# Optimization experiments

Hardware: AMD Instinct MI355X
Metric: run time of the kernel (lower is better)

Reference implementation:

```python
import jax, jax.numpy as jnp
import numpy as np

D_MODEL = 1024
N_HEADS = 16
DEPTH = D_MODEL // N_HEADS
B, S = 2, 2048
EPS_LN = 1e-6
EPS_KL = 2e-8


def _dense(x, W, b):
    return x @ W + b


def _ln(x, g, b):
    mu = jnp.mean(x, axis=-1, keepdims=True)
    var = jnp.mean(jnp.square(x - mu), axis=-1, keepdims=True)
    return (x - mu) * jax.lax.rsqrt(var + EPS_LN) * g + b


def _split_heads(x):
    # (B,S,D_MODEL) -> (B,H,S,DEPTH)
    return x.reshape(B, S, N_HEADS, DEPTH).transpose(0, 2, 1, 3)


def setup_inputs() -> dict:
    key = jax.random.key(0)
    ks = jax.random.split(key, 12)
    sc = 1.0 / np.sqrt(D_MODEL)
    inp = {
        'q_in': jax.random.normal(ks[0], (B, S, D_MODEL), jnp.float32),
        'k_in': jax.random.normal(ks[1], (B, S, D_MODEL), jnp.float32),
        'Wq': jax.random.normal(ks[2], (D_MODEL, D_MODEL), jnp.float32) * sc,
        'bq': jnp.zeros((D_MODEL,), jnp.float32),
        'Wk': jax.random.normal(ks[3], (D_MODEL, D_MODEL), jnp.float32) * sc,
        'bk': jnp.zeros((D_MODEL,), jnp.float32),
        'Wv': jax.random.normal(ks[4], (D_MODEL, D_MODEL), jnp.float32) * sc,
        'bv': jnp.zeros((D_MODEL,), jnp.float32),
        'Wo': jax.random.normal(ks[5], (D_MODEL, D_MODEL), jnp.float32) * sc,
        'bo': jnp.zeros((D_MODEL,), jnp.float32),
        'g1': jnp.ones((D_MODEL,), jnp.float32), 'b1': jnp.zeros((D_MODEL,), jnp.float32),
        'g2': jnp.ones((D_MODEL,), jnp.float32), 'b2': jnp.zeros((D_MODEL,), jnp.float32),
        'g3': jnp.ones((D_MODEL,), jnp.float32), 'b3': jnp.zeros((D_MODEL,), jnp.float32),
    }
    return inp


def reference(q_in, k_in, Wq, bq, Wk, bk, Wv, bv, Wo, bo, g1, b1, g2, b2, g3, b3):
    # Faithful to source: Wq applied twice to q, Wk twice to k, v = Wv(Wk(k_in))
    q = _ln(_dense(_dense(q_in, Wq, bq), Wq, bq), g1, b1)
    k1 = _dense(k_in, Wk, bk)
    k = _ln(_dense(k1, Wk, bk), g2, b2)
    v = _ln(_dense(k1, Wv, bv), g3, b3)

    q = _split_heads(q)   # (B,H,S,DEPTH)
    k = _split_heads(k)
    v = _split_heads(v)

    # KL-divergence attention scores.
    q_prob = jax.nn.softmax(q, axis=-1)
    k_prob = jax.nn.softmax(k, axis=-1)
    # sum_d q_prob*(log q_prob - log(k_prob+eps))
    # = [sum_d q_prob*log q_prob] - q_prob @ log(k_prob+eps)^T  (no 5D tensor)
    ent = jnp.sum(q_prob * jnp.log(q_prob), axis=-1)                     # (B,H,Sq)
    cross = jnp.einsum('bhqd,bhkd->bhqk', q_prob, jnp.log(k_prob + EPS_KL))
    kl_scores = ent[..., None] - cross                                   # (B,H,Sq,Sk)
    logits = kl_scores / jnp.sqrt(jnp.float32(DEPTH))

    # Csch softmax: csch(x)/sum csch(x)
    csch = 1.0 / jnp.sinh(logits)
    attn = csch / jnp.sum(csch, axis=-1, keepdims=True)                  # (B,H,Sq,Sk)

    out = jnp.einsum('bhqk,bhkd->bhqd', attn, v)
    out = out.transpose(0, 2, 1, 3).reshape(B, S, D_MODEL)
    output = _dense(out, Wo, bo)
    return output, attn
```

## Files before the change

kernel.cpp:

```cpp
#include <hip/hip_runtime.h>
#include <cstddef>
#include <cstdint>

#define BS      2
#define SEQ     2048
#define DM      1024
#define NH      16
#define DEPTH   64
#define ROWS    (BS*SEQ)
#define BHS     (BS*NH*SEQ)

typedef unsigned short u16;
typedef __attribute__((ext_vector_type(8))) short short8v;
typedef __attribute__((ext_vector_type(4))) float f32x4;

#define SWZ(row, cb) ((((row) << 7)) | ((cb) ^ (((row) & 7) << 4)))

__device__ __forceinline__ u16 f2bf(float x) {
    unsigned u = __builtin_bit_cast(unsigned, x);
    unsigned r = u + 0x7FFFu + ((u >> 16) & 1u);
    return (u16)(r >> 16);
}
__device__ __forceinline__ float bf2f(u16 h) {
    unsigned u = ((unsigned)h) << 16;
    return __builtin_bit_cast(float, u);
}

__device__ __forceinline__ float fast_csch(float x) {
    float t    = __expf(x);
    float den  = fmaf(t, t, -1.0f);
    bool  sm   = fabsf(x) < 0.04f;
    float d    = sm ? x : den;
    float r    = __builtin_amdgcn_rcpf(d);
    float big  = 2.0f * t * r;
    float smal = fmaf(x, -(1.0f/6.0f), r);
    return sm ? smal : big;
}

__global__ __launch_bounds__(256) void wsplit_kernel(
    const float* __restrict__ W, u16* __restrict__ H, u16* __restrict__ L)
{
    __shared__ float tile[32][33];
    const int bn = blockIdx.x, bk = blockIdx.y;
    const int c = threadIdx.x & 31, r0 = threadIdx.x >> 5;
#pragma unroll
    for (int r = 0; r < 32; r += 8)
        tile[r0 + r][c] = W[(size_t)(bk*32 + r0 + r) * DM + bn*32 + c];
    __syncthreads();
#pragma unroll
    for (int r = 0; r < 32; r += 8) {
        float v = tile[c][r0 + r];
        u16 h = f2bf(v);
        size_t o = (size_t)(bn*32 + r0 + r) * DM + bk*32 + c;
        H[o] = h;
        L[o] = f2bf(v - bf2f(h));
    }
}

__global__ __launch_bounds__(256) void split_kernel(
    const float* __restrict__ X, u16* __restrict__ H, u16* __restrict__ L)
{
    int i = blockIdx.x * 256 + threadIdx.x;
    float4 v = ((const float4*)X)[i];
    u16 h0 = f2bf(v.x), h1 = f2bf(v.y), h2 = f2bf(v.z), h3 = f2bf(v.w);
    u16 l0 = f2bf(v.x - bf2f(h0)), l1 = f2bf(v.y - bf2f(h1));
    u16 l2 = f2bf(v.z - bf2f(h2)), l3 = f2bf(v.w - bf2f(h3));
    uint2 hh, ll;
    hh.x = (unsigned)h0 | ((unsigned)h1 << 16); hh.y = (unsigned)h2 | ((unsigned)h3 << 16);
    ll.x = (unsigned)l0 | ((unsigned)l1 << 16); ll.y = (unsigned)l2 | ((unsigned)l3 << 16);
    ((uint2*)H)[i] = hh;
    ((uint2*)L)[i] = ll;
}

template<int OUT_MODE>
__global__ __launch_bounds__(256) void gemm_mfma(
    const u16* __restrict__ Ah, const u16* __restrict__ Al,
    const u16* __restrict__ Bh, const u16* __restrict__ Bl,
    const float* __restrict__ bias, float* __restrict__ C,
    u16* __restrict__ Ch, u16* __restrict__ Cl)
{
    constexpr int K = 1024, N = 1024;
    __shared__ u16 AsH[128*40], AsL[128*40], BsH[64*40], BsL[64*40];

    const int t = threadIdx.x;
    const int m0 = blockIdx.y * 128;
    const int n0 = blockIdx.x * 64;
    const int lane = t & 63, w = t >> 6;
    const int wr = w >> 1, wc = w & 1;
    const int lr = lane & 15, lk = lane >> 4;

    f32x4 acc[4][2];
#pragma unroll
    for (int i = 0; i < 4; ++i)
#pragma unroll
        for (int j = 0; j < 2; ++j) acc[i][j] = (f32x4){0.f,0.f,0.f,0.f};

    for (int k0 = 0; k0 < K; k0 += 32) {
        __syncthreads();
#pragma unroll
        for (int r = 0; r < 2; ++r) {
            int s = r*256 + t;
            int row = s >> 2, c = s & 3;
            size_t g = (size_t)(m0 + row) * K + k0 + c*8;
            *(short8v*)&AsH[row*40 + c*8] = *(const short8v*)&Ah[g];
            *(short8v*)&AsL[row*40 + c*8] = *(const short8v*)&Al[g];
        }
        {
            int row = t >> 2, c = t & 3;
            size_t g = (size_t)(n0 + row) * K + k0 + c*8;
            *(short8v*)&BsH[row*40 + c*8] = *(const short8v*)&Bh[g];
            *(short8v*)&BsL[row*40 + c*8] = *(const short8v*)&Bl[g];
        }
        __syncthreads();

        short8v ah[4], al[4], bh[2], bl[2];
#pragma unroll
        for (int i = 0; i < 4; ++i) {
            int off = (wr*64 + i*16 + lr)*40 + lk*8;
            ah[i] = *(const short8v*)&AsH[off];
            al[i] = *(const short8v*)&AsL[off];
        }
#pragma unroll
        for (int j = 0; j < 2; ++j) {
            int off = (wc*32 + j*16 + lr)*40 + lk*8;
            bh[j] = *(const short8v*)&BsH[off];
            bl[j] = *(const short8v*)&BsL[off];
        }
        __builtin_amdgcn_s_setprio(1);
#pragma unroll
        for (int i = 0; i < 4; ++i)
#pragma unroll
            for (int j = 0; j < 2; ++j) {
                acc[i][j] = __builtin_amdgcn_mfma_f32_16x16x32_bf16(ah[i], bh[j], acc[i][j], 0, 0, 0);
                acc[i][j] = __builtin_amdgcn_mfma_f32_16x16x32_bf16(ah[i], bl[j], acc[i][j], 0, 0, 0);
                acc[i][j] = __builtin_amdgcn_mfma_f32_16x16x32_bf16(al[i], bh[j], acc[i][j], 0, 0, 0);
            }
        __builtin_amdgcn_s_setprio(0);
    }

    float bj[2];
#pragma unroll
    for (int j = 0; j < 2; ++j) bj[j] = bias[n0 + wc*32 + j*16 + lr];
#pragma unroll
    for (int i = 0; i < 4; ++i)
#pragma unroll
        for (int j = 0; j < 2; ++j) {
            int col = n0 + wc*32 + j*16 + lr;
#pragma unroll
            for (int r = 0; r < 4; ++r) {
                int row = m0 + wr*64 + i*16 + lk*4 + r;
                float v = acc[i][j][r] + bj[j];
                size_t o = (size_t)row * N + col;
                if constexpr (OUT_MODE == 0) {
                    C[o] = v;
                } else {
                    u16 h = f2bf(v);
                    Ch[o] = h;
                    Cl[o] = f2bf(v - bf2f(h));
                }
            }
        }
}

template<int MODE>
__global__ __launch_bounds__(256) void ln_head_kernel(
    const float* __restrict__ X, const float* __restrict__ G,
    const float* __restrict__ Bt, u16* __restrict__ OA,
    u16* __restrict__ OB, float* __restrict__ ENT)
{
    const int row = blockIdx.x;
    const int tid = threadIdx.x;
    const float* x = X + (size_t)row * DM;
    float4 v = *(const float4*)&x[tid*4];

    float s  = v.x + v.y + v.z + v.w;
    float ss = v.x*v.x + v.y*v.y + v.z*v.z + v.w*v.w;
#pragma unroll
    for (int m = 1; m < 64; m <<= 1) { s += __shfl_xor(s, m); ss += __shfl_xor(ss, m); }
    __shared__ float redS[4], redQ[4];
    const int wave = tid >> 6, lane = tid & 63;
    if (lane == 0) { redS[wave] = s; redQ[wave] = ss; }
    __syncthreads();
    s  = redS[0] + redS[1] + redS[2] + redS[3];
    ss = redQ[0] + redQ[1] + redQ[2] + redQ[3];
    const float mu   = s * (1.0f / DM);
    const float var  = ss * (1.0f / DM) - mu * mu;
    const float rsig = rsqrtf(var + 1e-6f);

    float4 gv = *(const float4*)&G[tid*4];
    float4 bv = *(const float4*)&Bt[tid*4];
    float y0 = (v.x - mu) * rsig * gv.x + bv.x;
    float y1 = (v.y - mu) * rsig * gv.y + bv.y;
    float y2 = (v.z - mu) * rsig * gv.z + bv.z;
    float y3 = (v.w - mu) * rsig * gv.w + bv.w;

    const int b  = row >> 11;
    const int sl = row & (SEQ - 1);
    const int h  = tid >> 4;
    const size_t obase = (((size_t)(b*NH + h)) * SEQ + sl) * DEPTH + (tid & 15) * 4;

    if constexpr (MODE == 2) {
        unsigned w0 = (unsigned)f2bf(y0) | ((unsigned)f2bf(y1) << 16);
        unsigned w1 = (unsigned)f2bf(y2) | ((unsigned)f2bf(y3) << 16);
        *(uint2*)&OA[obase] = make_uint2(w0, w1);
    } else {
        float mx = fmaxf(fmaxf(y0, y1), fmaxf(y2, y3));
#pragma unroll
        for (int m = 1; m < 16; m <<= 1) mx = fmaxf(mx, __shfl_xor(mx, m, 16));
        float e0 = expf(y0 - mx), e1 = expf(y1 - mx), e2 = expf(y2 - mx), e3 = expf(y3 - mx);
        float se = e0 + e1 + e2 + e3;
#pragma unroll
        for (int m = 1; m < 16; m <<= 1) se += __shfl_xor(se, m, 16);
        float inv = 1.0f / se;
        float p0 = e0*inv, p1 = e1*inv, p2 = e2*inv, p3 = e3*inv;
        float o0, o1, o2, o3;
        if constexpr (MODE == 0) { o0 = p0; o1 = p1; o2 = p2; o3 = p3; }
        else {
            o0 = logf(p0 + 2e-8f); o1 = logf(p1 + 2e-8f);
            o2 = logf(p2 + 2e-8f); o3 = logf(p3 + 2e-8f);
        }
        u16 h0 = f2bf(o0), h1 = f2bf(o1), h2 = f2bf(o2), h3 = f2bf(o3);
        unsigned w0 = (unsigned)h0 | ((unsigned)h1 << 16);
        unsigned w1 = (unsigned)h2 | ((unsigned)h3 << 16);
        *(uint2*)&OA[obase] = make_uint2(w0, w1);
        u16 l0 = f2bf(o0 - bf2f(h0)), l1 = f2bf(o1 - bf2f(h1));
        u16 l2 = f2bf(o2 - bf2f(h2)), l3 = f2bf(o3 - bf2f(h3));
        w0 = (unsigned)l0 | ((unsigned)l1 << 16);
        w1 = (unsigned)l2 | ((unsigned)l3 << 16);
        *(uint2*)&OB[obase] = make_uint2(w0, w1);

        if constexpr (MODE == 0) {
            float lse = logf(se);
            float el = p0*(y0-mx-lse) + p1*(y1-mx-lse) + p2*(y2-mx-lse) + p3*(y3-mx-lse);
#pragma unroll
            for (int m = 1; m < 16; m <<= 1) el += __shfl_xor(el, m, 16);
            if ((tid & 15) == 0) ENT[((size_t)(b*NH + h)) * SEQ + sl] = el;
        }
    }
}

__global__ __launch_bounds__(256) void vtrans_kernel(
    const u16* __restrict__ Vb, u16* __restrict__ VT)
{
    __shared__ u16 T[256*72];
    const int bh = blockIdx.y;
    const int s0 = blockIdx.x * 256;
    const int t  = threadIdx.x;
#pragma unroll
    for (int i = 0; i < 8; ++i) {
        int c = i*256 + t;
        int s = c >> 3, d0 = (c & 7) * 8;
        *(short8v*)&T[s*72 + d0] =
            *(const short8v*)&Vb[((size_t)bh*SEQ + s0 + s)*DEPTH + d0];
    }
    __syncthreads();
#pragma unroll
    for (int i = 0; i < 8; ++i) {
        int c = i*256 + t;
        int d = c >> 5, sl0 = (c & 31) * 8;
        short8v v;
#pragma unroll
        for (int j = 0; j < 8; ++j) v[j] = (short)T[(sl0 + j)*72 + d];
        *(short8v*)&VT[((size_t)bh*DEPTH + d)*SEQ + s0 + sl0] = v;
    }
}

__global__ __launch_bounds__(256, 4) void attn5_kernel(
    const u16* __restrict__ QPh, const u16* __restrict__ QPl,
    const u16* __restrict__ LKh, const u16* __restrict__ LKl,
    const u16* __restrict__ VT, const float* __restrict__ ENT,
    float* __restrict__ ATTN, u16* __restrict__ OH, u16* __restrict__ OL)
{
    const int wg   = blockIdx.x;
    const int wgid = (wg & 7) * 128 + (wg >> 3);
    const int bh   = wgid >> 5;
    const int q0   = (wgid & 31) * 64;

    const int t  = threadIdx.x;
    const int l  = t & 63, w = t >> 6;
    const int lr = l & 15, lg = l >> 4;
    const size_t rbase = (size_t)bh * SEQ;

    __shared__ u16 KhS[64*64], KlS[64*64], VtS[64*64], PS[64*64];

    short8v qh[2], ql[2];
#pragma unroll
    for (int d = 0; d < 2; ++d) {
        size_t g = (rbase + q0 + w*16 + lr) * DEPTH + d*32 + lg*8;
        qh[d] = *(const short8v*)&QPh[g];
        ql[d] = *(const short8v*)&QPl[g];
    }
    float e8[4];
#pragma unroll
    for (int r = 0; r < 4; ++r)
        e8[r] = ENT[rbase + q0 + w*16 + lg*4 + r] * 0.125f;

    float rs[4] = {0.f, 0.f, 0.f, 0.f};
    for (int k0 = 0; k0 < SEQ; k0 += 64) {
        if (k0) __syncthreads();
#pragma unroll
        for (int r = 0; r < 2; ++r) {
            int s = r*256 + t; int kr = s >> 3, cb = (s & 7) * 16;
            size_t g = (rbase + k0 + kr) * DEPTH + (s & 7) * 8;
            *(short8v*)((char*)KhS + SWZ(kr, cb)) = *(const short8v*)&LKh[g];
            *(short8v*)((char*)KlS + SWZ(kr, cb)) = *(const short8v*)&LKl[g];
        }
        __syncthreads();

        f32x4 acc[4];
#pragma unroll
        for (int f = 0; f < 4; ++f) acc[f] = (f32x4){0.f,0.f,0.f,0.f};
        __builtin_amdgcn_s_setprio(1);
#pragma unroll
        for (int f = 0; f < 4; ++f)
#pragma unroll
            for (int d = 0; d < 2; ++d) {
                int off = SWZ(f*16 + lr, d*64 + lg*16);
                short8v kbh = *(const short8v*)((const char*)KhS + off);
                short8v kbl = *(const short8v*)((const char*)KlS + off);
                acc[f] = __builtin_amdgcn_mfma_f32_16x16x32_bf16(qh[d], kbh, acc[f], 0, 0, 0);
                acc[f] = __builtin_amdgcn_mfma_f32_16x16x32_bf16(qh[d], kbl, acc[f], 0, 0, 0);
                acc[f] = __builtin_amdgcn_mfma_f32_16x16x32_bf16(ql[d], kbh, acc[f], 0, 0, 0);
            }
        __builtin_amdgcn_s_setprio(0);
#pragma unroll
        for (int f = 0; f < 4; ++f)
#pragma unroll
            for (int r = 0; r < 4; ++r)
                rs[r] += fast_csch(fmaf(acc[f][r], -0.125f, e8[r]));
    }
#pragma unroll
    for (int m = 1; m < 16; m <<= 1)
#pragma unroll
        for (int r = 0; r < 4; ++r) rs[r] += __shfl_xor(rs[r], m, 16);
    float inv[4];
#pragma unroll
    for (int r = 0; r < 4; ++r) inv[r] = 1.0f / rs[r];

    f32x4 av[4];
#pragma unroll
    for (int nf = 0; nf < 4; ++nf) av[nf] = (f32x4){0.f,0.f,0.f,0.f};

    for (int k0 = 0; k0 < SEQ; k0 += 64) {
        __syncthreads();
#pragma unroll
        for (int r = 0; r < 2; ++r) {
            int s = r*256 + t; int kr = s >> 3, cb = (s & 7) * 16;
            size_t g = (rbase + k0 + kr) * DEPTH + (s & 7) * 8;
            *(short8v*)((char*)KhS + SWZ(kr, cb)) = *(const short8v*)&LKh[g];
            *(short8v*)((char*)KlS + SWZ(kr, cb)) = *(const short8v*)&LKl[g];
        }
#pragma unroll
        for (int r = 0; r < 2; ++r) {
            int s = r*256 + t; int dd = s >> 3, cb = (s & 7) * 16;
            *(short8v*)((char*)VtS + SWZ(dd, cb)) =
                *(const short8v*)&VT[((size_t)bh * DEPTH + dd) * SEQ + k0 + (s & 7) * 8];
        }
        __syncthreads();

        f32x4 acc[4];
#pragma unroll
        for (int f = 0; f < 4; ++f) acc[f] = (f32x4){0.f,0.f,0.f,0.f};
        __builtin_amdgcn_s_setprio(1);
#pragma unroll
        for (int f = 0; f < 4; ++f)
#pragma unroll
            for (int d = 0; d < 2; ++d) {
                int off = SWZ(f*16 + lr, d*64 + lg*16);
                short8v kbh = *(const short8v*)((const char*)KhS + off);
                short8v kbl = *(const short8v*)((const char*)KlS + off);
                acc[f] = __builtin_amdgcn_mfma_f32_16x16x32_bf16(qh[d], kbh, acc[f], 0, 0, 0);
                acc[f] = __builtin_amdgcn_mfma_f32_16x16x32_bf16(qh[d], kbl, acc[f], 0, 0, 0);
                acc[f] = __builtin_amdgcn_mfma_f32_16x16x32_bf16(ql[d], kbh, acc[f], 0, 0, 0);
            }
        __builtin_amdgcn_s_setprio(0);

#pragma unroll
        for (int f = 0; f < 4; ++f)
#pragma unroll
            for (int r = 0; r < 4; ++r) {
                float c = fast_csch(fmaf(acc[f][r], -0.125f, e8[r]));
                float a = c * inv[r];
                int q = w*16 + lg*4 + r;
                ATTN[(rbase + q0 + q) * SEQ + k0 + f*16 + lr] = a;
                *(u16*)((char*)PS + SWZ(q, (f*16 + lr)*2)) = f2bf(a);
            }

        short8v pa[2];
#pragma unroll
        for (int ks = 0; ks < 2; ++ks)
            pa[ks] = *(const short8v*)((const char*)PS + SWZ(w*16 + lr, ks*64 + lg*16));
        __builtin_amdgcn_s_setprio(1);
#pragma unroll
        for (int nf = 0; nf < 4; ++nf)
#pragma unroll
            for (int ks = 0; ks < 2; ++ks) {
                short8v vb = *(const short8v*)((const char*)VtS + SWZ(nf*16 + lr, ks*64 + lg*16));
                av[nf] = __builtin_amdgcn_mfma_f32_16x16x32_bf16(pa[ks], vb, av[nf], 0, 0, 0);
            }
        __builtin_amdgcn_s_setprio(0);
    }

    const int b = bh >> 4, h = bh & (NH - 1);
#pragma unroll
    for (int nf = 0; nf < 4; ++nf)
#pragma unroll
        for (int r = 0; r < 4; ++r) {
            int q = w*16 + lg*4 + r;
            int d = nf*16 + lr;
            size_t o = ((size_t)(b * SEQ + q0 + q)) * DM + h * DEPTH + d;
            float v = av[nf][r];
            u16 hh = f2bf(v);
            OH[o] = hh;
            OL[o] = f2bf(v - bf2f(hh));
        }
}

extern "C" void kernel_launch(void* const* d_in, const int* in_sizes, int n_in,
                              void* d_out, int out_size, void* d_ws, size_t ws_size,
                              hipStream_t stream)
{
    const float* q_in = (const float*)d_in[0];
    const float* k_in = (const float*)d_in[1];
    const float* Wq = (const float*)d_in[2];
    const float* bq = (const float*)d_in[3];
    const float* Wk = (const float*)d_in[4];
    const float* bk = (const float*)d_in[5];
    const float* Wv = (const float*)d_in[6];
    const float* bvp = (const float*)d_in[7];
    const float* Wo = (const float*)d_in[8];
    const float* bo = (const float*)d_in[9];
    const float* g1 = (const float*)d_in[10];
    const float* b1 = (const float*)d_in[11];
    const float* g2 = (const float*)d_in[12];
    const float* b2 = (const float*)d_in[13];
    const float* g3 = (const float*)d_in[14];
    const float* b3 = (const float*)d_in[15];

    float* out0 = (float*)d_out;
    float* attn = out0 + (size_t)ROWS * DM;

    char* base = (char*)d_ws;
    const size_t SLOT = (size_t)ROWS * DM * 4;
    const size_t HALF = (size_t)ROWS * DM;
    float* S0f = (float*)(base);
    float* S1f = (float*)(base + SLOT);
    float* S2f = (float*)(base + 2*SLOT);
    float* S3f = (float*)(base + 3*SLOT);
    u16* S0h = (u16*)S0f; u16* S0l = S0h + HALF;
    u16* S1h = (u16*)S1f; u16* S1l = S1h + HALF;
    u16* S3h = (u16*)S3f; u16* S3l = S3h + HALF;
    u16* QPh = (u16*)S3f; u16* QPl = QPh + HALF;
    u16* LKh = (u16*)S2f; u16* LKl = LKh + HALF;
    u16* Vb  = (u16*)S0f; u16* VTp = Vb + HALF;
    u16* OHp = (u16*)S1f; u16* OLp = OHp + HALF;

    char* wbase = base + 4*SLOT;
    const size_t WSZ = (size_t)DM * DM * 2;
    u16* WqH = (u16*)(wbase);           u16* WqL = (u16*)(wbase + WSZ);
    u16* WkH = (u16*)(wbase + 2*WSZ);   u16* WkL = (u16*)(wbase + 3*WSZ);
    u16* WvH = (u16*)(wbase + 4*WSZ);   u16* WvL = (u16*)(wbase + 5*WSZ);
    u16* WoH = (u16*)(wbase + 6*WSZ);   u16* WoL = (u16*)(wbase + 7*WSZ);
    float* ent = (float*)(wbase + 8*WSZ);

    const dim3 wgrid(32, 32);
    const dim3 ggrid(DM/64, ROWS/128);

    wsplit_kernel<<<wgrid, 256, 0, stream>>>(Wq, WqH, WqL);
    wsplit_kernel<<<wgrid, 256, 0, stream>>>(Wk, WkH, WkL);
    wsplit_kernel<<<wgrid, 256, 0, stream>>>(Wv, WvH, WvL);
    wsplit_kernel<<<wgrid, 256, 0, stream>>>(Wo, WoH, WoL);

    split_kernel<<<ROWS*DM/(4*256), 256, 0, stream>>>(q_in, S0h, S0l);
    gemm_mfma<1><<<ggrid, 256, 0, stream>>>(S0h, S0l, WqH, WqL, bq, nullptr, S1h, S1l);
    gemm_mfma<0><<<ggrid, 256, 0, stream>>>(S1h, S1l, WqH, WqL, bq, S2f, nullptr, nullptr);
    split_kernel<<<ROWS*DM/(4*256), 256, 0, stream>>>(k_in, S0h, S0l);
    gemm_mfma<1><<<ggrid, 256, 0, stream>>>(S0h, S0l, WkH, WkL, bk, nullptr, S3h, S3l);
    gemm_mfma<0><<<ggrid, 256, 0, stream>>>(S3h, S3l, WkH, WkL, bk, S0f, nullptr, nullptr);
    gemm_mfma<0><<<ggrid, 256, 0, stream>>>(S3h, S3l, WvH, WvL, bvp, S1f, nullptr, nullptr);

    ln_head_kernel<0><<<ROWS, 256, 0, stream>>>(S2f, g1, b1, QPh, QPl, ent);
    ln_head_kernel<1><<<ROWS, 256, 0, stream>>>(S0f, g2, b2, LKh, LKl, nullptr);
    ln_head_kernel<2><<<ROWS, 256, 0, stream>>>(S1f, g3, b3, Vb, nullptr, nullptr);
    vtrans_kernel<<<dim3(SEQ/256, BS*NH), 256, 0, stream>>>(Vb, VTp);

    attn5_kernel<<<dim3(SEQ/64 * BS*NH), 256, 0, stream>>>(
        QPh, QPl, LKh, LKl, VTp, ent, attn, OHp, OLp);

    gemm_mfma<0><<<ggrid, 256, 0, stream>>>(OHp, OLp, WoH, WoL, bo, out0, nullptr, nullptr);
}
```

Baseline: 581.2 us.

## Precompose Wq·Wq, fuse input splitting into GEMM, prefetch attention K/V tiles

Computes Wq@Wq and the folded bias once, so the double q projection becomes a single GEMM over a 1024x1024 weight product. A new GEMM variant loads fp32 activations and splits them into bf16 hi/lo inside the kernel, which removes the separate split passes. The four weight-split launches are merged into one launch, and the attention kernel now prefetches the next K/Kl/V tile into registers while computing the current one. In exchange it adds a small GEMM and a bias kernel, raises register pressure in attention, and changes rounding order in the q path.

```diff
diff --git a/kernel.cpp b/kernel.cpp
--- a/kernel.cpp
+++ b/kernel.cpp
@@ -37,9 +37,19 @@
     return sm ? smal : big;
 }
 
-__global__ __launch_bounds__(256) void wsplit_kernel(
-    const float* __restrict__ W, u16* __restrict__ H, u16* __restrict__ L)
-{
+__global__ __launch_bounds__(256) void wsplit4_kernel(
+    const float* __restrict__ W0, const float* __restrict__ W1,
+    const float* __restrict__ W2_, const float* __restrict__ W3,
+    u16* __restrict__ H0, u16* __restrict__ L0, u16* __restrict__ H1, u16* __restrict__ L1,
+    u16* __restrict__ H2, u16* __restrict__ L2, u16* __restrict__ H3, u16* __restrict__ L3)
+{
+    const float* W; u16* H; u16* L;
+    switch (blockIdx.z) {
+        case 0: W = W0; H = H0; L = L0; break;
+        case 1: W = W1; H = H1; L = L1; break;
+        case 2: W = W2_; H = H2; L = L2; break;
+        default: W = W3; H = H3; L = L3; break;
+    }
     __shared__ float tile[32][33];
     const int bn = blockIdx.x, bk = blockIdx.y;
     const int c = threadIdx.x & 31, r0 = threadIdx.x >> 5;
@@ -72,6 +82,25 @@
     ((uint2*)L)[i] = ll;
 }
 
+__global__ __launch_bounds__(256) void bias2_kernel(
+    const float* __restrict__ bq, const float* __restrict__ Wq,
+    float* __restrict__ bq2)
+{
+    __shared__ float part[4][64];
+    const int t = threadIdx.x;
+    const int nl = t & 63, kk = t >> 6;
+    const int n = blockIdx.x * 64 + nl;
+    float acc = 0.0f;
+#pragma unroll 8
+    for (int k = kk*256; k < kk*256 + 256; ++k)
+        acc = fmaf(bq[k], Wq[(size_t)k * DM + n], acc);
+    part[kk][nl] = acc;
+    __syncthreads();
+    if (t < 64)
+        bq2[blockIdx.x*64 + t] = part[0][t] + part[1][t] + part[2][t] + part[3][t]
+                               + bq[blockIdx.x*64 + t];
+}
+
 template<int OUT_MODE>
 __global__ __launch_bounds__(256) void gemm_mfma(
     const u16* __restrict__ Ah, const u16* __restrict__ Al,
@@ -140,7 +169,7 @@
 
     float bj[2];
 #pragma unroll
-    for (int j = 0; j < 2; ++j) bj[j] = bias[n0 + wc*32 + j*16 + lr];
+    for (int j = 0; j < 2; ++j) bj[j] = bias ? bias[n0 + wc*32 + j*16 + lr] : 0.0f;
 #pragma unroll
     for (int i = 0; i < 4; ++i)
 #pragma unroll
@@ -162,6 +191,106 @@
         }
 }
 
+template<int OUT_MODE>
+__global__ __launch_bounds__(256) void gemm_f32a(
+    const float* __restrict__ A,
+    const u16* __restrict__ Bh, const u16* __restrict__ Bl,
+    const float* __restrict__ bias, float* __restrict__ C,
+    u16* __restrict__ Ch, u16* __restrict__ Cl)
+{
+    constexpr int K = 1024, N = 1024;
+    __shared__ u16 AsH[128*40], AsL[128*40], BsH[64*40], BsL[64*40];
+
+    const int t = threadIdx.x;
+    const int m0 = blockIdx.y * 128;
+    const int n0 = blockIdx.x * 64;
+    const int lane = t & 63, w = t >> 6;
+    const int wr = w >> 1, wc = w & 1;
+    const int lr = lane & 15, lk = lane >> 4;
+
+    f32x4 acc[4][2];
+#pragma unroll
+    for (int i = 0; i < 4; ++i)
+#pragma unroll
+        for (int j = 0; j < 2; ++j) acc[i][j] = (f32x4){0.f,0.f,0.f,0.f};
+
+    for (int k0 = 0; k0 < K; k0 += 32) {
+        __syncthreads();
+#pragma unroll
+        for (int r = 0; r < 2; ++r) {
+            int j = r*256 + t;
+            int row = j >> 2, c8 = j & 3;
+            const float* src = &A[(size_t)(m0 + row) * K + k0 + c8*8];
+            float4 a = *(const float4*)src;
+            float4 b = *(const float4*)(src + 4);
+            float xs[8] = {a.x,a.y,a.z,a.w,b.x,b.y,b.z,b.w};
+            short8v hv, lv;
+#pragma unroll
+            for (int jj = 0; jj < 8; ++jj) {
+                u16 h = f2bf(xs[jj]);
+                hv[jj] = (short)h;
+                lv[jj] = (short)f2bf(xs[jj] - bf2f(h));
+            }
+            *(short8v*)&AsH[row*40 + c8*8] = hv;
+            *(short8v*)&AsL[row*40 + c8*8] = lv;
+        }
+        {
+            int row = t >> 2, c = t & 3;
+            size_t g = (size_t)(n0 + row) * K + k0 + c*8;
+            *(short8v*)&BsH[row*40 + c*8] = *(const short8v*)&Bh[g];
+            *(short8v*)&BsL[row*40 + c*8] = *(const short8v*)&Bl[g];
+        }
+        __syncthreads();
+
+        short8v ah[4], al[4], bh[2], bl[2];
+#pragma unroll
+        for (int i = 0; i < 4; ++i) {
+            int off = (wr*64 + i*16 + lr)*40 + lk*8;
+            ah[i] = *(const short8v*)&AsH[off];
+            al[i] = *(const short8v*)&AsL[off];
+        }
+#pragma unroll
+        for (int j = 0; j < 2; ++j) {
+            int off = (wc*32 + j*16 + lr)*40 + lk*8;
+            bh[j] = *(const short8v*)&BsH[off];
+            bl[j] = *(const short8v*)&BsL[off];
+        }
+        __builtin_amdgcn_s_setprio(1);
+#pragma unroll
+        for (int i = 0; i < 4; ++i)
+#pragma unroll
+            for (int j = 0; j < 2; ++j) {
+                acc[i][j] = __builtin_amdgcn_mfma_f32_16x16x32_bf16(ah[i], bh[j], acc[i][j], 0, 0, 0);
+                acc[i][j] = __builtin_amdgcn_mfma_f32_16x16x32_bf16(ah[i], bl[j], acc[i][j], 0, 0, 0);
+                acc[i][j] = __builtin_amdgcn_mfma_f32_16x16x32_bf16(al[i], bh[j], acc[i][j], 0, 0, 0);
+            }
+        __builtin_amdgcn_s_setprio(0);
+    }
+
+    float bj[2];
+#pragma unroll
+    for (int j = 0; j < 2; ++j) bj[j] = bias ? bias[n0 + wc*32 + j*16 + lr] : 0.0f;
+#pragma unroll
+    for (int i = 0; i < 4; ++i)
+#pragma unroll
+        for (int j = 0; j < 2; ++j) {
+            int col = n0 + wc*32 + j*16 + lr;
+#pragma unroll
+            for (int r = 0; r < 4; ++r) {
+                int row = m0 + wr*64 + i*16 + lk*4 + r;
+                float v = acc[i][j][r] + bj[j];
+                size_t o = (size_t)row * N + col;
+                if constexpr (OUT_MODE == 0) {
+                    C[o] = v;
+                } else {
+                    u16 h = f2bf(v);
+                    Ch[o] = h;
+                    Cl[o] = f2bf(v - bf2f(h));
+                }
+            }
+        }
+}
+
 template<int MODE>
 __global__ __launch_bounds__(256) void ln_head_kernel(
     const float* __restrict__ X, const float* __restrict__ G,
@@ -265,7 +394,7 @@
     }
 }
 
-__global__ __launch_bounds__(256, 4) void attn5_kernel(
+__global__ __launch_bounds__(256, 4) void attn6_kernel(
     const u16* __restrict__ QPh, const u16* __restrict__ QPl,
     const u16* __restrict__ LKh, const u16* __restrict__ LKl,
     const u16* __restrict__ VT, const float* __restrict__ ENT,
@@ -283,6 +412,10 @@
 
     __shared__ u16 KhS[64*64], KlS[64*64], VtS[64*64], PS[64*64];
 
+    const int kr0 = t >> 3,           c0 = t & 7;
+    const int kr1 = (256 + t) >> 3,   c1 = t & 7;
+    const int wz0 = SWZ(kr0, c0*16), wz1 = SWZ(kr1, c1*16);
+
     short8v qh[2], ql[2];
 #pragma unroll
     for (int d = 0; d < 2; ++d) {
@@ -295,17 +428,26 @@
     for (int r = 0; r < 4; ++r)
         e8[r] = ENT[rbase + q0 + w*16 + lg*4 + r] * 0.125f;
 
+    {
+        size_t g0 = (rbase + kr0) * DEPTH + c0*8;
+        size_t g1 = (rbase + kr1) * DEPTH + c1*8;
+        *(short8v*)((char*)KhS + wz0) = *(const short8v*)&LKh[g0];
+        *(short8v*)((char*)KlS + wz0) = *(const short8v*)&LKl[g0];
+        *(short8v*)((char*)KhS + wz1) = *(const short8v*)&LKh[g1];
+        *(short8v*)((char*)KlS + wz1) = *(const short8v*)&LKl[g1];
+    }
+    __syncthreads();
+
     float rs[4] = {0.f, 0.f, 0.f, 0.f};
     for (int k0 = 0; k0 < SEQ; k0 += 64) {
-        if (k0) __syncthreads();
-#pragma unroll
-        for (int r = 0; r < 2; ++r) {
-            int s = r*256 + t; int kr = s >> 3, cb = (s & 7) * 16;
-            size_t g = (rbase + k0 + kr) * DEPTH + (s & 7) * 8;
-            *(short8v*)((char*)KhS + SWZ(kr, cb)) = *(const short8v*)&LKh[g];
-            *(short8v*)((char*)KlS + SWZ(kr, cb)) = *(const short8v*)&LKl[g];
-        }
-        __syncthreads();
+        const bool more = (k0 + 64) < SEQ;
+        short8v ph0, pl0, ph1, pl1;
+        if (more) {
+            size_t g0 = (rbase + k0 + 64 + kr0) * DEPTH + c0*8;
+            size_t g1 = (rbase + k0 + 64 + kr1) * DEPTH + c1*8;
+            ph0 = *(const short8v*)&LKh[g0]; pl0 = *(const short8v*)&LKl[g0];
+            ph1 = *(const short8v*)&LKh[g1]; pl1 = *(const short8v*)&LKl[g1];
+        }
 
         f32x4 acc[4];
 #pragma unroll
@@ -328,6 +470,15 @@
 #pragma unroll
             for (int r = 0; r < 4; ++r)
                 rs[r] += fast_csch(fmaf(acc[f][r], -0.125f, e8[r]));
+
+        __syncthreads();
+        if (more) {
+            *(short8v*)((char*)KhS + wz0) = ph0;
+            *(short8v*)((char*)KlS + wz0) = pl0;
+            *(short8v*)((char*)KhS + wz1) = ph1;
+            *(short8v*)((char*)KlS + wz1) = pl1;
+            __syncthreads();
+        }
     }
 #pragma unroll
     for (int m = 1; m < 16; m <<= 1)
@@ -337,26 +488,37 @@
 #pragma unroll
     for (int r = 0; r < 4; ++r) inv[r] = 1.0f / rs[r];
 
+    {
+        size_t g0 = (rbase + kr0) * DEPTH + c0*8;
+        size_t g1 = (rbase + kr1) * DEPTH + c1*8;
+        *(short8v*)((char*)KhS + wz0) = *(const short8v*)&LKh[g0];
+        *(short8v*)((char*)KlS + wz0) = *(const short8v*)&LKl[g0];
+        *(short8v*)((char*)KhS + wz1) = *(const short8v*)&LKh[g1];
+        *(short8v*)((char*)KlS + wz1) = *(const short8v*)&LKl[g1];
+        size_t v0 = ((size_t)bh * DEPTH + kr0) * SEQ + c0*8;
+        size_t v1 = ((size_t)bh * DEPTH + kr1) * SEQ + c1*8;
+        *(short8v*)((char*)VtS + wz0) = *(const short8v*)&VT[v0];
+        *(short8v*)((char*)VtS + wz1) = *(const short8v*)&VT[v1];
+    }
+    __syncthreads();
+
     f32x4 av[4];
 #pragma unroll
     for (int nf = 0; nf < 4; ++nf) av[nf] = (f32x4){0.f,0.f,0.f,0.f};
 
     for (int k0 = 0; k0 < SEQ; k0 += 64) {
-        __syncthreads();
-#pragma unroll
-        for (int r = 0; r < 2; ++r) {
-            int s = r*256 + t; int kr = s >> 3, cb = (s & 7) * 16;
-            size_t g = (rbase + k0 + kr) * DEPTH + (s & 7) * 8;
-            *(short8v*)((char*)KhS + SWZ(kr, cb)) = *(const short8v*)&LKh[g];
-            *(short8v*)((char*)KlS + SWZ(kr, cb)) = *(const short8v*)&LKl[g];
-        }
-#pragma unroll
-        for (int r = 0; r < 2; ++r) {
-            int s = r*256 + t; int dd = s >> 3, cb = (s & 7) * 16;
-            *(short8v*)((char*)VtS + SWZ(dd, cb)) =
-                *(const short8v*)&VT[((size_t)bh * DEPTH + dd) * SEQ + k0 + (s & 7) * 8];
-        }
-        __syncthreads();
+        const bool more = (k0 + 64) < SEQ;
+        short8v ph0, pl0, ph1, pl1, pv0, pv1;
+        if (more) {
+            size_t g0 = (rbase + k0 + 64 + kr0) * DEPTH + c0*8;
+            size_t g1 = (rbase + k0 + 64 + kr1) * DEPTH + c1*8;
+            ph0 = *(const short8v*)&LKh[g0]; pl0 = *(const short8v*)&LKl[g0];
+            ph1 = *(const short8v*)&LKh[g1]; pl1 = *(const short8v*)&LKl[g1];
+            size_t v0 = ((size_t)bh * DEPTH + kr0) * SEQ + k0 + 64 + c0*8;
+            size_t v1 = ((size_t)bh * DEPTH + kr1) * SEQ + k0 + 64 + c1*8;
+            pv0 = *(const short8v*)&VT[v0];
+            pv1 = *(const short8v*)&VT[v1];
+        }
 
         f32x4 acc[4];
 #pragma unroll
@@ -399,6 +561,17 @@
                 av[nf] = __builtin_amdgcn_mfma_f32_16x16x32_bf16(pa[ks], vb, av[nf], 0, 0, 0);
             }
         __builtin_amdgcn_s_setprio(0);
+
+        __syncthreads();
+        if (more) {
+            *(short8v*)((char*)KhS + wz0) = ph0;
+            *(short8v*)((char*)KlS + wz0) = pl0;
+            *(short8v*)((char*)KhS + wz1) = ph1;
+            *(short8v*)((char*)KlS + wz1) = pl1;
+            *(short8v*)((char*)VtS + wz0) = pv0;
+            *(short8v*)((char*)VtS + wz1) = pv1;
+            __syncthreads();
+        }
     }
 
     const int b = bh >> 4, h = bh & (NH - 1);
@@ -448,12 +621,14 @@
     float* S2f = (float*)(base + 2*SLOT);
     float* S3f = (float*)(base + 3*SLOT);
     u16* S0h = (u16*)S0f; u16* S0l = S0h + HALF;
-    u16* S1h = (u16*)S1f; u16* S1l = S1h + HALF;
+    u16* S1h = (u16*)S1f;
     u16* S3h = (u16*)S3f; u16* S3l = S3h + HALF;
     u16* QPh = (u16*)S3f; u16* QPl = QPh + HALF;
     u16* LKh = (u16*)S2f; u16* LKl = LKh + HALF;
     u16* Vb  = (u16*)S0f; u16* VTp = Vb + HALF;
     u16* OHp = (u16*)S1f; u16* OLp = OHp + HALF;
+    u16* WqnH = S0h;
+    u16* WqnL = S0h + (size_t)DM*DM;
 
     char* wbase = base + 4*SLOT;
     const size_t WSZ = (size_t)DM * DM * 2;
@@ -461,21 +636,22 @@
     u16* WkH = (u16*)(wbase + 2*WSZ);   u16* WkL = (u16*)(wbase + 3*WSZ);
     u16* WvH = (u16*)(wbase + 4*WSZ);   u16* WvL = (u16*)(wbase + 5*WSZ);
     u16* WoH = (u16*)(wbase + 6*WSZ);   u16* WoL = (u16*)(wbase + 7*WSZ);
-    float* ent = (float*)(wbase + 8*WSZ);
-
-    const dim3 wgrid(32, 32);
+    u16* W2H = (u16*)(wbase + 8*WSZ);   u16* W2L = (u16*)(wbase + 9*WSZ);
+    float* ent = (float*)(wbase + 10*WSZ);
+    float* bq2 = ent + BHS;
+
     const dim3 ggrid(DM/64, ROWS/128);
-
-    wsplit_kernel<<<wgrid, 256, 0, stream>>>(Wq, WqH, WqL);
-    wsplit_kernel<<<wgrid, 256, 0, stream>>>(Wk, WkH, WkL);
-    wsplit_kernel<<<wgrid, 256, 0, stream>>>(Wv, WvH, WvL);
-    wsplit_kernel<<<wgrid, 256, 0, stream>>>(Wo, WoH, WoL);
-
-    split_kernel<<<ROWS*DM/(4*256), 256, 0, stream>>>(q_in, S0h, S0l);
-    gemm_mfma<1><<<ggrid, 256, 0, stream>>>(S0h, S0l, WqH, WqL, bq, nullptr, S1h, S1l);
-    gemm_mfma<0><<<ggrid, 256, 0, stream>>>(S1h, S1l, WqH, WqL, bq, S2f, nullptr, nullptr);
-    split_kernel<<<ROWS*DM/(4*256), 256, 0, stream>>>(k_in, S0h, S0l);
-    gemm_mfma<1><<<ggrid, 256, 0, stream>>>(S0h, S0l, WkH, WkL, bk, nullptr, S3h, S3l);
+    const dim3 g2grid(DM/64, DM/128);
+
+    wsplit4_kernel<<<dim3(32,32,4), 256, 0, stream>>>(
+        Wq, Wk, Wv, Wo, WqH, WqL, WkH, WkL, WvH, WvL, WoH, WoL);
+    split_kernel<<<DM*DM/(4*256), 256, 0, stream>>>(Wq, WqnH, WqnL);
+    bias2_kernel<<<16, 256, 0, stream>>>(bq, Wq, bq2);
+    gemm_mfma<1><<<g2grid, 256, 0, stream>>>(WqH, WqL, WqnH, WqnL, nullptr,
+                                             nullptr, W2H, W2L);
+
+    gemm_f32a<0><<<ggrid, 256, 0, stream>>>(q_in, W2H, W2L, bq2, S2f, nullptr, nullptr);
+    gemm_f32a<1><<<ggrid, 256, 0, stream>>>(k_in, WkH, WkL, bk, nullptr, S3h, S3l);
     gemm_mfma<0><<<ggrid, 256, 0, stream>>>(S3h, S3l, WkH, WkL, bk, S0f, nullptr, nullptr);
     gemm_mfma<0><<<ggrid, 256, 0, stream>>>(S3h, S3l, WvH, WvL, bvp, S1f, nullptr, nullptr);
 
@@ -484,7 +660,7 @@
     ln_head_kernel<2><<<ROWS, 256, 0, stream>>>(S1f, g3, b3, Vb, nullptr, nullptr);
     vtrans_kernel<<<dim3(SEQ/256, BS*NH), 256, 0, stream>>>(Vb, VTp);
 
-    attn5_kernel<<<dim3(SEQ/64 * BS*NH), 256, 0, stream>>>(
+    attn6_kernel<<<dim3(SEQ/64 * BS*NH), 256, 0, stream>>>(
         QPh, QPl, LKh, LKl, VTp, ent, attn, OHp, OLp);
 
     gemm_mfma<0><<<ggrid, 256, 0, stream>>>(OHp, OLp, WoH, WoL, bo, out0, nullptr, nullptr);
```

Result: slower. 605.1 us (+4.1%).
